# Performance work log

Hardware: AMD Instinct MI355X
Metric: run time of the kernel (lower is better)

## Reference

```python
import jax, jax.numpy as jnp
import numpy as np

N_NODES = 100000
FEAT = 64
HID = 128
N_EDGES = 1200000


def setup_inputs() -> dict:
    key = jax.random.key(0)
    ks = jax.random.split(key, 8)
    x = jax.random.normal(ks[0], (N_NODES, FEAT), dtype=jnp.float32)
    edge_index = jax.random.randint(ks[1], (2, N_EDGES), 0, N_NODES, dtype=jnp.int32)
    # SAGEConv params: lin_l (on aggregated neighbors, with bias), lin_r (on root, no bias)
    W1l = jax.random.normal(ks[2], (HID, FEAT), jnp.float32) / np.float32(np.sqrt(FEAT))
    b1l = jnp.zeros((HID,), jnp.float32)
    W1r = jax.random.normal(ks[3], (HID, FEAT), jnp.float32) / np.float32(np.sqrt(FEAT))
    W2l = jax.random.normal(ks[4], (FEAT, HID), jnp.float32) / np.float32(np.sqrt(HID))
    b2l = jnp.zeros((FEAT,), jnp.float32)
    W2r = jax.random.normal(ks[5], (FEAT, HID), jnp.float32) / np.float32(np.sqrt(HID))
    return {"x": x, "edge_index": edge_index, "W1l": W1l, "b1l": b1l,
            "W1r": W1r, "W2l": W2l, "b2l": b2l, "W2r": W2r}


def _sage_conv(x, src, dst, Wl, bl, Wr, n_nodes):
    # mean aggregation of neighbor messages x[src] at targets dst
    msg = x[src]                                                  # [E, d]
    agg = jax.ops.segment_sum(msg, dst, num_segments=n_nodes)     # [N, d]
    deg = jax.ops.segment_sum(jnp.ones((src.shape[0],), x.dtype), dst,
                              num_segments=n_nodes)               # [N]
    agg = agg / jnp.maximum(deg, 1.0)[:, None]
    # out = lin_l(agg) + lin_r(x); lin_r has no bias (PyG SAGEConv default)
    return agg @ Wl.T + bl + x @ Wr.T


def reference(x, edge_index, W1l, b1l, W1r, W2l, b2l, W2r):
    src, dst = edge_index[0], edge_index[1]
    n = x.shape[0]
    h = jax.nn.relu(_sage_conv(x, src, dst, W1l, b1l, W1r, n))
    # dropout(p=0.5) is identity in eval mode
    out = _sage_conv(h, src, dst, W2l, b2l, W2r, n)
    return out
```

## Files before the change

### kernel.cpp

```cpp
#include <hip/hip_runtime.h>
#include <hip/hip_bf16.h>

typedef __bf16 bf16;
typedef __attribute__((ext_vector_type(8))) __bf16 bf16x8;
typedef __attribute__((ext_vector_type(4))) __bf16 bf16x4;
typedef __attribute__((ext_vector_type(4))) float f32x4;

#define NBLK 256

__device__ inline void unpack8(uint4 r, f32x4& a, f32x4& b) {
  a.x = __uint_as_float(r.x << 16);
  a.y = __uint_as_float(r.x & 0xffff0000u);
  a.z = __uint_as_float(r.y << 16);
  a.w = __uint_as_float(r.y & 0xffff0000u);
  b.x = __uint_as_float(r.z << 16);
  b.y = __uint_as_float(r.z & 0xffff0000u);
  b.z = __uint_as_float(r.w << 16);
  b.w = __uint_as_float(r.w & 0xffff0000u);
}

__device__ inline uint4 slot_load(const bf16* __restrict__ tab, const int* __restrict__ nbr,
                                  int base, int e, int q, int fo) {
  int idx = base + q;
  uint4 r = make_uint4(0u, 0u, 0u, 0u);
  if (idx < e) {
    int j = nbr[idx];
    r = *(const uint4*)(tab + j * 64 + fo);
  }
  return r;
}

__global__ __launch_bounds__(256) void setup_k(const float* __restrict__ x,
                                               const int* __restrict__ dst,
                                               const float* __restrict__ W1l,
                                               const float* __restrict__ W1r,
                                               const float* __restrict__ W2l,
                                               const float* __restrict__ W2r,
                                               bf16* __restrict__ xb,
                                               bf16* __restrict__ B1,
                                               bf16* __restrict__ B2,
                                               int* __restrict__ hist,
                                               int E, int nb, int N, int Np) {
  __shared__ int h[1024];
  int t = threadIdx.x;
  if (blockIdx.x < NBLK) {
    for (int i = t; i < nb; i += 256) h[i] = 0;
    __syncthreads();
    int chunk = (E + NBLK - 1) / NBLK;
    int s = blockIdx.x * chunk, e = min(E, s + chunk);
    for (int i = s + t; i < e; i += 256) atomicAdd(&h[dst[i] >> 7], 1);
    __syncthreads();
    for (int i = t; i < nb; i += 256) hist[(long)i * NBLK + blockIdx.x] = h[i];
  } else if (blockIdx.x < NBLK + 128) {
    int gid = (blockIdx.x - NBLK) * 256 + t;
    if (gid < 16384) {
      int c = gid >> 7, k = gid & 127;
      float v = (k < 64) ? W1l[c * 64 + k] : W1r[c * 64 + (k - 64)];
      B1[gid] = (bf16)v;
    } else {
      int idx = gid - 16384;
      int n = idx >> 7, k = idx & 127;
      float v = (n < 64) ? W2l[n * 128 + k] : W2r[(n - 64) * 128 + k];
      B2[idx] = (bf16)v;
    }
  } else {
    int gid = (blockIdx.x - NBLK - 128) * 256 + t;
    long base = (long)gid * 4;
    if (base >= (long)Np * 64) return;
    if (base < (long)N * 64) {
      f32x4 v = *(const f32x4*)(x + base);
      bf16 o[4] = {(bf16)v.x, (bf16)v.y, (bf16)v.z, (bf16)v.w};
      *(ulong1*)(xb + base) = *(ulong1*)o;
    } else {
      bf16 o[4] = {(bf16)0.0f, (bf16)0.0f, (bf16)0.0f, (bf16)0.0f};
      *(ulong1*)(xb + base) = *(ulong1*)o;
    }
  }
}

__global__ __launch_bounds__(256) void scanA_k(int* __restrict__ hist,
                                               int* __restrict__ bsum, int M) {
  __shared__ int sd[256];
  int t = threadIdx.x;
  int idx = blockIdx.x * 256 + t;
  int v = (idx < M) ? hist[idx] : 0;
  sd[t] = v;
  __syncthreads();
#pragma unroll
  for (int off = 1; off < 256; off <<= 1) {
    int tv = (t >= off) ? sd[t - off] : 0;
    __syncthreads();
    if (t >= off) sd[t] += tv;
    __syncthreads();
  }
  if (idx < M) hist[idx] = sd[t] - v;
  if (t == 255) bsum[blockIdx.x] = sd[255];
}

__global__ __launch_bounds__(1024) void scanB_k(int* __restrict__ bsum, int NB2) {
  __shared__ int sd[1024];
  int t = threadIdx.x;
  int v = (t < NB2) ? bsum[t] : 0;
  sd[t] = v;
  __syncthreads();
#pragma unroll
  for (int off = 1; off < 1024; off <<= 1) {
    int tv = (t >= off) ? sd[t - off] : 0;
    __syncthreads();
    if (t >= off) sd[t] += tv;
    __syncthreads();
  }
  if (t < NB2) bsum[t] = sd[t] - v;
}

__global__ __launch_bounds__(256) void scanC_k(int* __restrict__ hist,
                                               const int* __restrict__ bsum,
                                               int* __restrict__ boff,
                                               int M, int nb, int E) {
  int idx = blockIdx.x * 256 + threadIdx.x;
  if (idx >= M) return;
  int v = hist[idx] + bsum[idx >> 8];
  hist[idx] = v;
  if ((idx & (NBLK - 1)) == 0) boff[idx / NBLK] = v;
  if (idx == 0) boff[nb] = E;
}

__global__ __launch_bounds__(512) void scat_k(const int* __restrict__ src,
                                              const int* __restrict__ dst,
                                              const int* __restrict__ hist,
                                              unsigned* __restrict__ ebuf, int E, int nb) {
  __shared__ int cur[1024];
  for (int i = threadIdx.x; i < nb; i += 512)
    cur[i] = hist[(long)i * NBLK + blockIdx.x];
  __syncthreads();
  int chunk = (E + NBLK - 1) / NBLK;
  int s = blockIdx.x * chunk, e = min(E, s + chunk);
  for (int i = s + threadIdx.x; i < e; i += 512) {
    int d = dst[i];
    int pos = atomicAdd(&cur[d >> 7], 1);
    ebuf[pos] = ((unsigned)src[i] << 7) | (unsigned)(d & 127);
  }
}

__global__ __launch_bounds__(256) void csr_k(const unsigned* __restrict__ ebuf,
                                             const int* __restrict__ boff,
                                             int* __restrict__ rowptr,
                                             int* __restrict__ nbr, int Np, int E) {
  __shared__ int hcnt[128];
  __shared__ int hoff[128];
  int b = blockIdx.x, t = threadIdx.x;
  int s = boff[b], e = boff[b + 1];
  if (t < 128) hcnt[t] = 0;
  __syncthreads();
  for (int i = s + t; i < e; i += 256) atomicAdd(&hcnt[ebuf[i] & 127u], 1);
  __syncthreads();
  if (t < 128) hoff[t] = hcnt[t];
  __syncthreads();
#pragma unroll
  for (int off = 1; off < 128; off <<= 1) {
    int v = (t < 128 && t >= off) ? hoff[t - off] : 0;
    __syncthreads();
    if (t < 128 && t >= off) hoff[t] += v;
    __syncthreads();
  }
  if (t < 128) {
    int ex = hoff[t] - hcnt[t];
    rowptr[b * 128 + t] = s + ex;
    hcnt[t] = ex;
  }
  if (blockIdx.x == gridDim.x - 1 && t == 0) rowptr[Np] = E;
  __syncthreads();
  for (int i = s + t; i < e; i += 256) {
    unsigned r = ebuf[i];
    int pos = atomicAdd(&hcnt[r & 127u], 1);
    nbr[s + pos] = (int)(r >> 7);
  }
}

__global__ __launch_bounds__(256) void agg1_k(const bf16* __restrict__ xb,
                                              const int* __restrict__ rowptr,
                                              const int* __restrict__ nbr,
                                              bf16* __restrict__ A1, int Np) {
  int wave = threadIdx.x >> 6, lane = threadIdx.x & 63;
  int n = blockIdx.x * 4 + wave;
  if (n >= Np) return;
  int s = rowptr[n], e = rowptr[n + 1];
  int q = lane >> 3, f = lane & 7;
  int fo = f * 8;
  f32x4 sa = {0, 0, 0, 0}, sb = {0, 0, 0, 0};
  uint4 c0 = slot_load(xb, nbr, s, e, q, fo);
  uint4 c1 = slot_load(xb, nbr, s + 8, e, q, fo);
  int i = s + 16;
  for (; i < e; i += 16) {
    uint4 n0 = slot_load(xb, nbr, i, e, q, fo);
    uint4 n1 = slot_load(xb, nbr, i + 8, e, q, fo);
    f32x4 a, b;
    unpack8(c0, a, b); sa += a; sb += b;
    unpack8(c1, a, b); sa += a; sb += b;
    c0 = n0; c1 = n1;
  }
  {
    f32x4 a, b;
    unpack8(c0, a, b); sa += a; sb += b;
    unpack8(c1, a, b); sa += a; sb += b;
  }
  float v[8] = {sa.x, sa.y, sa.z, sa.w, sb.x, sb.y, sb.z, sb.w};
#pragma unroll
  for (int k = 0; k < 8; k++) {
    v[k] += __shfl_xor(v[k], 8);
    v[k] += __shfl_xor(v[k], 16);
    v[k] += __shfl_xor(v[k], 32);
  }
  float invd = 1.0f / fmaxf((float)(e - s), 1.0f);
  if (q == 0) {
    bf16x8 o = {(bf16)(v[0] * invd), (bf16)(v[1] * invd), (bf16)(v[2] * invd),
                (bf16)(v[3] * invd), (bf16)(v[4] * invd), (bf16)(v[5] * invd),
                (bf16)(v[6] * invd), (bf16)(v[7] * invd)};
    *(bf16x8*)(A1 + n * 128 + fo) = o;
  } else if (q == 1) {
    uint4 rv = *(const uint4*)(xb + n * 64 + fo);
    *(uint4*)(A1 + n * 128 + 64 + fo) = rv;
  }
}

__global__ __launch_bounds__(256) void gemm_bf16_k(const bf16* __restrict__ A,
                                                   const bf16* __restrict__ B,
                                                   bf16* __restrict__ Ct,
                                                   bf16* __restrict__ Cu,
                                                   const float* __restrict__ bias,
                                                   int relu) {
  int wave = threadIdx.x >> 6;
  int lane = threadIdx.x & 63;
  int row = lane & 15;
  int quad = lane >> 4;
  long mbase = (long)blockIdx.x * 128 + (long)wave * 32;

  bf16x8 bfrag[8][4];
#pragma unroll
  for (int j = 0; j < 8; j++)
#pragma unroll
    for (int s = 0; s < 4; s++)
      bfrag[j][s] = *(const bf16x8*)(B + (long)(j * 16 + row) * 128 + s * 32 + quad * 8);

  f32x4 acc[2][8] = {};
#pragma unroll
  for (int s = 0; s < 4; s++) {
    bf16x8 a0 = *(const bf16x8*)(A + (mbase + row) * 128 + s * 32 + quad * 8);
    bf16x8 a1 = *(const bf16x8*)(A + (mbase + 16 + row) * 128 + s * 32 + quad * 8);
#pragma unroll
    for (int j = 0; j < 8; j++) {
      acc[0][j] = __builtin_amdgcn_mfma_f32_16x16x32_bf16(a0, bfrag[j][s], acc[0][j], 0, 0, 0);
      acc[1][j] = __builtin_amdgcn_mfma_f32_16x16x32_bf16(a1, bfrag[j][s], acc[1][j], 0, 0, 0);
    }
  }

#pragma unroll
  for (int r = 0; r < 2; r++) {
    long rb = mbase + r * 16;
#pragma unroll
    for (int j = 0; j < 8; j++) {
      int col = j * 16 + row;
      float bv = bias ? bias[col] : 0.0f;
#pragma unroll
      for (int i = 0; i < 4; i++) {
        float v = acc[r][j][i] + bv;
        if (relu) v = v > 0.0f ? v : 0.0f;
        long mrow = rb + quad * 4 + i;
        if (Cu) {
          if (col < 64) Ct[mrow * 64 + col] = (bf16)v;
          else Cu[mrow * 64 + (col - 64)] = (bf16)v;
        } else {
          Ct[mrow * 128 + col] = (bf16)v;
        }
      }
    }
  }
}

__global__ __launch_bounds__(256) void agg2_k(const bf16* __restrict__ tmat,
                                              const bf16* __restrict__ umat,
                                              const int* __restrict__ rowptr,
                                              const int* __restrict__ nbr,
                                              const float* __restrict__ b2l,
                                              float* __restrict__ out, int N) {
  int wave = threadIdx.x >> 6, lane = threadIdx.x & 63;
  int n = blockIdx.x * 4 + wave;
  if (n >= N) return;
  int s = rowptr[n], e = rowptr[n + 1];
  int q = lane >> 3, f = lane & 7;
  int fo = f * 8;
  f32x4 sa = {0, 0, 0, 0}, sb = {0, 0, 0, 0};
  uint4 c0 = slot_load(tmat, nbr, s, e, q, fo);
  uint4 c1 = slot_load(tmat, nbr, s + 8, e, q, fo);
  int i = s + 16;
  for (; i < e; i += 16) {
    uint4 n0 = slot_load(tmat, nbr, i, e, q, fo);
    uint4 n1 = slot_load(tmat, nbr, i + 8, e, q, fo);
    f32x4 a, b;
    unpack8(c0, a, b); sa += a; sb += b;
    unpack8(c1, a, b); sa += a; sb += b;
    c0 = n0; c1 = n1;
  }
  {
    f32x4 a, b;
    unpack8(c0, a, b); sa += a; sb += b;
    unpack8(c1, a, b); sa += a; sb += b;
  }
  float v[8] = {sa.x, sa.y, sa.z, sa.w, sb.x, sb.y, sb.z, sb.w};
#pragma unroll
  for (int k = 0; k < 8; k++) {
    v[k] += __shfl_xor(v[k], 8);
    v[k] += __shfl_xor(v[k], 16);
    v[k] += __shfl_xor(v[k], 32);
  }
  if (q == 0) {
    float invd = 1.0f / fmaxf((float)(e - s), 1.0f);
    f32x4 b0 = *(const f32x4*)(b2l + fo);
    f32x4 b1 = *(const f32x4*)(b2l + fo + 4);
    f32x4 ua, ub;
    unpack8(*(const uint4*)(umat + n * 64 + fo), ua, ub);
    f32x4 o0, o1;
    o0.x = v[0] * invd + b0.x + ua.x;
    o0.y = v[1] * invd + b0.y + ua.y;
    o0.z = v[2] * invd + b0.z + ua.z;
    o0.w = v[3] * invd + b0.w + ua.w;
    o1.x = v[4] * invd + b1.x + ub.x;
    o1.y = v[5] * invd + b1.y + ub.y;
    o1.z = v[6] * invd + b1.z + ub.z;
    o1.w = v[7] * invd + b1.w + ub.w;
    *(f32x4*)(out + n * 64 + fo) = o0;
    *(f32x4*)(out + n * 64 + fo + 4) = o1;
  }
}

static inline size_t align256(size_t x) { return (x + 255) / 256 * 256; }

extern "C" void kernel_launch(void* const* d_in, const int* in_sizes, int n_in,
                              void* d_out, int out_size, void* d_ws, size_t ws_size,
                              hipStream_t stream) {
  const float* x = (const float*)d_in[0];
  const int* edge_index = (const int*)d_in[1];
  const float* W1l = (const float*)d_in[2];
  const float* b1l = (const float*)d_in[3];
  const float* W1r = (const float*)d_in[4];
  const float* W2l = (const float*)d_in[5];
  const float* b2l = (const float*)d_in[6];
  const float* W2r = (const float*)d_in[7];

  const int N = in_sizes[0] / 64;
  const int E = in_sizes[1] / 2;
  const int Np = (N + 127) / 128 * 128;
  const int nb = Np / 128;
  const int M = nb * NBLK;
  const int NB2 = (M + 255) / 256;

  const int* src = edge_index;
  const int* dst = edge_index + E;

  char* ws = (char*)d_ws;
  size_t off = 0;
  int* hist = (int*)(ws + off);         off += align256((size_t)M * 4);
  int* bsum = (int*)(ws + off);         off += align256((size_t)NB2 * 4);
  int* boff = (int*)(ws + off);         off += align256((size_t)(nb + 1) * 4);
  int* rowptr = (int*)(ws + off);       off += align256((size_t)(Np + 1) * 4);
  unsigned* ebuf = (unsigned*)(ws + off); off += align256((size_t)E * 4);
  int* nbr = (int*)(ws + off);          off += align256((size_t)E * 4);
  bf16* xb = (bf16*)(ws + off);         off += align256((size_t)Np * 64 * 2);
  bf16* A1 = (bf16*)(ws + off);
  bf16* tmat = (bf16*)(ws + off);       off += align256((size_t)Np * 64 * 2);
  bf16* umat = (bf16*)(ws + off);       off += align256((size_t)Np * 64 * 2);
  bf16* h = (bf16*)(ws + off);          off += align256((size_t)Np * 128 * 2);
  bf16* B1 = (bf16*)(ws + off);         off += align256(128 * 128 * 2);
  bf16* B2 = (bf16*)(ws + off);         off += align256(128 * 128 * 2);
  float* out = (float*)d_out;

  const int cvtBlocks = (int)(((long)Np * 64 / 4 + 255) / 256);
  setup_k<<<NBLK + 128 + cvtBlocks, 256, 0, stream>>>(x, dst, W1l, W1r, W2l, W2r,
                                                      xb, B1, B2, hist, E, nb, N, Np);
  scanA_k<<<NB2, 256, 0, stream>>>(hist, bsum, M);
  scanB_k<<<1, 1024, 0, stream>>>(bsum, NB2);
  scanC_k<<<(M + 255) / 256, 256, 0, stream>>>(hist, bsum, boff, M, nb, E);
  scat_k<<<NBLK, 512, 0, stream>>>(src, dst, hist, ebuf, E, nb);
  csr_k<<<nb, 256, 0, stream>>>(ebuf, boff, rowptr, nbr, Np, E);

  agg1_k<<<Np / 4, 256, 0, stream>>>(xb, rowptr, nbr, A1, Np);
  gemm_bf16_k<<<Np / 128, 256, 0, stream>>>(A1, B1, h, nullptr, b1l, 1);
  gemm_bf16_k<<<Np / 128, 256, 0, stream>>>(h, B2, tmat, umat, nullptr, 0);
  agg2_k<<<(N + 3) / 4, 256, 0, stream>>>(tmat, umat, rowptr, nbr, b2l, out, N);
}
```

Measured before the change: 263.7 us.

## Fuse two layer GEMMs via LDS and fold scan fixup into consumers

Merges the two per-layer GEMMs into one kernel that keeps the ReLU hidden tile in shared memory, removing the global write and re-read of the hidden matrix and one launch. The scan now uses one block per node bucket, so block sums alone give bucket offsets; the separate fixup kernel is dropped and scatter/CSR add the block offset themselves. B fragments are now loaded per step inside the loop instead of being preloaded into registers, trading register pressure for more repeated global/L1 loads. The hidden tile also uses extra LDS, which may lower occupancy.

New measurement: 251.5 us. 1.05x faster.

```diff
diff --git a/kernel.cpp b/kernel.cpp
--- a/kernel.cpp
+++ b/kernel.cpp
@@ -3,7 +3,6 @@
 
 typedef __bf16 bf16;
 typedef __attribute__((ext_vector_type(8))) __bf16 bf16x8;
-typedef __attribute__((ext_vector_type(4))) __bf16 bf16x4;
 typedef __attribute__((ext_vector_type(4))) float f32x4;
 
 #define NBLK 256
@@ -79,11 +78,11 @@
 }
 
 __global__ __launch_bounds__(256) void scanA_k(int* __restrict__ hist,
-                                               int* __restrict__ bsum, int M) {
+                                               int* __restrict__ bsum) {
   __shared__ int sd[256];
   int t = threadIdx.x;
   int idx = blockIdx.x * 256 + t;
-  int v = (idx < M) ? hist[idx] : 0;
+  int v = hist[idx];
   sd[t] = v;
   __syncthreads();
 #pragma unroll
@@ -93,14 +92,14 @@
     if (t >= off) sd[t] += tv;
     __syncthreads();
   }
-  if (idx < M) hist[idx] = sd[t] - v;
+  hist[idx] = sd[t] - v;
   if (t == 255) bsum[blockIdx.x] = sd[255];
 }
 
-__global__ __launch_bounds__(1024) void scanB_k(int* __restrict__ bsum, int NB2) {
+__global__ __launch_bounds__(1024) void scanB_k(int* __restrict__ bsum, int nb) {
   __shared__ int sd[1024];
   int t = threadIdx.x;
-  int v = (t < NB2) ? bsum[t] : 0;
+  int v = (t < nb) ? bsum[t] : 0;
   sd[t] = v;
   __syncthreads();
 #pragma unroll
@@ -110,28 +109,17 @@
     if (t >= off) sd[t] += tv;
     __syncthreads();
   }
-  if (t < NB2) bsum[t] = sd[t] - v;
-}
-
-__global__ __launch_bounds__(256) void scanC_k(int* __restrict__ hist,
-                                               const int* __restrict__ bsum,
-                                               int* __restrict__ boff,
-                                               int M, int nb, int E) {
-  int idx = blockIdx.x * 256 + threadIdx.x;
-  if (idx >= M) return;
-  int v = hist[idx] + bsum[idx >> 8];
-  hist[idx] = v;
-  if ((idx & (NBLK - 1)) == 0) boff[idx / NBLK] = v;
-  if (idx == 0) boff[nb] = E;
+  if (t < nb) bsum[t] = sd[t] - v;
 }
 
 __global__ __launch_bounds__(512) void scat_k(const int* __restrict__ src,
                                               const int* __restrict__ dst,
                                               const int* __restrict__ hist,
+                                              const int* __restrict__ bsum,
                                               unsigned* __restrict__ ebuf, int E, int nb) {
   __shared__ int cur[1024];
   for (int i = threadIdx.x; i < nb; i += 512)
-    cur[i] = hist[(long)i * NBLK + blockIdx.x];
+    cur[i] = bsum[i] + hist[(long)i * NBLK + blockIdx.x];
   __syncthreads();
   int chunk = (E + NBLK - 1) / NBLK;
   int s = blockIdx.x * chunk, e = min(E, s + chunk);
@@ -143,13 +131,14 @@
 }
 
 __global__ __launch_bounds__(256) void csr_k(const unsigned* __restrict__ ebuf,
-                                             const int* __restrict__ boff,
+                                             const int* __restrict__ bsum,
                                              int* __restrict__ rowptr,
-                                             int* __restrict__ nbr, int Np, int E) {
+                                             int* __restrict__ nbr, int nb, int Np, int E) {
   __shared__ int hcnt[128];
   __shared__ int hoff[128];
   int b = blockIdx.x, t = threadIdx.x;
-  int s = boff[b], e = boff[b + 1];
+  int s = bsum[b];
+  int e = (b + 1 < nb) ? bsum[b + 1] : E;
   if (t < 128) hcnt[t] = 0;
   __syncthreads();
   for (int i = s + t; i < e; i += 256) atomicAdd(&hcnt[ebuf[i] & 127u], 1);
@@ -223,24 +212,19 @@
   }
 }
 
-__global__ __launch_bounds__(256) void gemm_bf16_k(const bf16* __restrict__ A,
-                                                   const bf16* __restrict__ B,
-                                                   bf16* __restrict__ Ct,
-                                                   bf16* __restrict__ Cu,
-                                                   const float* __restrict__ bias,
-                                                   int relu) {
+__global__ __launch_bounds__(256) void gemm2x_k(const bf16* __restrict__ A,
+                                                const bf16* __restrict__ B1,
+                                                const bf16* __restrict__ B2,
+                                                const float* __restrict__ b1l,
+                                                bf16* __restrict__ Ct,
+                                                bf16* __restrict__ Cu) {
+  __shared__ bf16 hl[128][136];
   int wave = threadIdx.x >> 6;
   int lane = threadIdx.x & 63;
   int row = lane & 15;
   int quad = lane >> 4;
   long mbase = (long)blockIdx.x * 128 + (long)wave * 32;
-
-  bf16x8 bfrag[8][4];
-#pragma unroll
-  for (int j = 0; j < 8; j++)
-#pragma unroll
-    for (int s = 0; s < 4; s++)
-      bfrag[j][s] = *(const bf16x8*)(B + (long)(j * 16 + row) * 128 + s * 32 + quad * 8);
+  int mloc = wave * 32;
 
   f32x4 acc[2][8] = {};
 #pragma unroll
@@ -249,29 +233,51 @@
     bf16x8 a1 = *(const bf16x8*)(A + (mbase + 16 + row) * 128 + s * 32 + quad * 8);
 #pragma unroll
     for (int j = 0; j < 8; j++) {
-      acc[0][j] = __builtin_amdgcn_mfma_f32_16x16x32_bf16(a0, bfrag[j][s], acc[0][j], 0, 0, 0);
-      acc[1][j] = __builtin_amdgcn_mfma_f32_16x16x32_bf16(a1, bfrag[j][s], acc[1][j], 0, 0, 0);
-    }
-  }
-
+      bf16x8 bf = *(const bf16x8*)(B1 + (long)(j * 16 + row) * 128 + s * 32 + quad * 8);
+      acc[0][j] = __builtin_amdgcn_mfma_f32_16x16x32_bf16(a0, bf, acc[0][j], 0, 0, 0);
+      acc[1][j] = __builtin_amdgcn_mfma_f32_16x16x32_bf16(a1, bf, acc[1][j], 0, 0, 0);
+    }
+  }
+#pragma unroll
+  for (int r = 0; r < 2; r++) {
+#pragma unroll
+    for (int j = 0; j < 8; j++) {
+      int col = j * 16 + row;
+      float bv = b1l[col];
+#pragma unroll
+      for (int i = 0; i < 4; i++) {
+        float v = acc[r][j][i] + bv;
+        v = v > 0.0f ? v : 0.0f;
+        hl[mloc + r * 16 + quad * 4 + i][col] = (bf16)v;
+      }
+    }
+  }
+  __syncthreads();
+
+  f32x4 acc2[2][8] = {};
+#pragma unroll
+  for (int s = 0; s < 4; s++) {
+    bf16x8 a0 = *(const bf16x8*)(&hl[mloc + row][s * 32 + quad * 8]);
+    bf16x8 a1 = *(const bf16x8*)(&hl[mloc + 16 + row][s * 32 + quad * 8]);
+#pragma unroll
+    for (int j = 0; j < 8; j++) {
+      bf16x8 bf = *(const bf16x8*)(B2 + (long)(j * 16 + row) * 128 + s * 32 + quad * 8);
+      acc2[0][j] = __builtin_amdgcn_mfma_f32_16x16x32_bf16(a0, bf, acc2[0][j], 0, 0, 0);
+      acc2[1][j] = __builtin_amdgcn_mfma_f32_16x16x32_bf16(a1, bf, acc2[1][j], 0, 0, 0);
+    }
+  }
 #pragma unroll
   for (int r = 0; r < 2; r++) {
     long rb = mbase + r * 16;
 #pragma unroll
     for (int j = 0; j < 8; j++) {
       int col = j * 16 + row;
-      float bv = bias ? bias[col] : 0.0f;
 #pragma unroll
       for (int i = 0; i < 4; i++) {
-        float v = acc[r][j][i] + bv;
-        if (relu) v = v > 0.0f ? v : 0.0f;
+        float v = acc2[r][j][i];
         long mrow = rb + quad * 4 + i;
-        if (Cu) {
-          if (col < 64) Ct[mrow * 64 + col] = (bf16)v;
-          else Cu[mrow * 64 + (col - 64)] = (bf16)v;
-        } else {
-          Ct[mrow * 128 + col] = (bf16)v;
-        }
+        if (col < 64) Ct[mrow * 64 + col] = (bf16)v;
+        else Cu[mrow * 64 + (col - 64)] = (bf16)v;
       }
     }
   }
@@ -352,39 +358,34 @@
   const int Np = (N + 127) / 128 * 128;
   const int nb = Np / 128;
   const int M = nb * NBLK;
-  const int NB2 = (M + 255) / 256;
 
   const int* src = edge_index;
   const int* dst = edge_index + E;
 
   char* ws = (char*)d_ws;
   size_t off = 0;
-  int* hist = (int*)(ws + off);         off += align256((size_t)M * 4);
-  int* bsum = (int*)(ws + off);         off += align256((size_t)NB2 * 4);
-  int* boff = (int*)(ws + off);         off += align256((size_t)(nb + 1) * 4);
-  int* rowptr = (int*)(ws + off);       off += align256((size_t)(Np + 1) * 4);
+  int* hist = (int*)(ws + off);           off += align256((size_t)M * 4);
+  int* bsum = (int*)(ws + off);           off += align256((size_t)nb * 4);
+  int* rowptr = (int*)(ws + off);         off += align256((size_t)(Np + 1) * 4);
   unsigned* ebuf = (unsigned*)(ws + off); off += align256((size_t)E * 4);
-  int* nbr = (int*)(ws + off);          off += align256((size_t)E * 4);
-  bf16* xb = (bf16*)(ws + off);         off += align256((size_t)Np * 64 * 2);
-  bf16* A1 = (bf16*)(ws + off);
-  bf16* tmat = (bf16*)(ws + off);       off += align256((size_t)Np * 64 * 2);
-  bf16* umat = (bf16*)(ws + off);       off += align256((size_t)Np * 64 * 2);
-  bf16* h = (bf16*)(ws + off);          off += align256((size_t)Np * 128 * 2);
-  bf16* B1 = (bf16*)(ws + off);         off += align256(128 * 128 * 2);
-  bf16* B2 = (bf16*)(ws + off);         off += align256(128 * 128 * 2);
+  int* nbr = (int*)(ws + off);            off += align256((size_t)E * 4);
+  bf16* xb = (bf16*)(ws + off);           off += align256((size_t)Np * 64 * 2);
+  bf16* A1 = (bf16*)(ws + off);           off += align256((size_t)Np * 128 * 2);
+  bf16* tmat = (bf16*)(ws + off);         off += align256((size_t)Np * 64 * 2);
+  bf16* umat = (bf16*)(ws + off);         off += align256((size_t)Np * 64 * 2);
+  bf16* B1 = (bf16*)(ws + off);           off += align256(128 * 128 * 2);
+  bf16* B2 = (bf16*)(ws + off);           off += align256(128 * 128 * 2);
   float* out = (float*)d_out;
 
   const int cvtBlocks = (int)(((long)Np * 64 / 4 + 255) / 256);
   setup_k<<<NBLK + 128 + cvtBlocks, 256, 0, stream>>>(x, dst, W1l, W1r, W2l, W2r,
                                                       xb, B1, B2, hist, E, nb, N, Np);
-  scanA_k<<<NB2, 256, 0, stream>>>(hist, bsum, M);
-  scanB_k<<<1, 1024, 0, stream>>>(bsum, NB2);
-  scanC_k<<<(M + 255) / 256, 256, 0, stream>>>(hist, bsum, boff, M, nb, E);
-  scat_k<<<NBLK, 512, 0, stream>>>(src, dst, hist, ebuf, E, nb);
-  csr_k<<<nb, 256, 0, stream>>>(ebuf, boff, rowptr, nbr, Np, E);
+  scanA_k<<<nb, 256, 0, stream>>>(hist, bsum);
+  scanB_k<<<1, 1024, 0, stream>>>(bsum, nb);
+  scat_k<<<NBLK, 512, 0, stream>>>(src, dst, hist, bsum, ebuf, E, nb);
+  csr_k<<<nb, 256, 0, stream>>>(ebuf, bsum, rowptr, nbr, nb, Np, E);
 
   agg1_k<<<Np / 4, 256, 0, stream>>>(xb, rowptr, nbr, A1, Np);
-  gemm_bf16_k<<<Np / 128, 256, 0, stream>>>(A1, B1, h, nullptr, b1l, 1);
-  gemm_bf16_k<<<Np / 128, 256, 0, stream>>>(h, B2, tmat, umat, nullptr, 0);
+  gemm2x_k<<<Np / 128, 256, 0, stream>>>(A1, B1, B2, b1l, tmat, umat);
   agg2_k<<<(N + 3) / 4, 256, 0, stream>>>(tmat, umat, rowptr, nbr, b2l, out, N);
 }
```
